# Performance work log

Hardware: AMD Instinct MI355X
Metric: run time of the kernel (lower is better)

## Reference

```python
import jax, jax.numpy as jnp
import numpy as np

B, T, I, H, V = 128, 1024, 256, 512, 32000


def setup_inputs() -> dict:
    key = jax.random.key(0)
    ks = jax.random.split(key, 16)
    s = lambda fan_in: 1.0 / np.sqrt(fan_in)
    return {
        "x": jax.random.normal(ks[0], (B, 1, I), jnp.float32),
        "hp": jax.random.normal(ks[1], (1, B, H), jnp.float32),
        "cp": jax.random.normal(ks[2], (1, B, H), jnp.float32),
        "op": jax.random.normal(ks[3], (B, H), jnp.float32),
        "encoder_outputs": jax.random.normal(ks[4], (B, T, H), jnp.float32),
        # LSTM params (PyTorch gate order: i, f, g, o)
        "W_ih": jax.random.uniform(ks[5], (4 * H, I + H), jnp.float32, -s(H), s(H)),
        "W_hh": jax.random.uniform(ks[6], (4 * H, H), jnp.float32, -s(H), s(H)),
        "b_ih": jax.random.uniform(ks[7], (4 * H,), jnp.float32, -s(H), s(H)),
        "b_hh": jax.random.uniform(ks[8], (4 * H,), jnp.float32, -s(H), s(H)),
        # Bahdanau attention (all bias-free)
        "Wq": jax.random.uniform(ks[9], (H, H), jnp.float32, -s(H), s(H)),
        "Wm": jax.random.uniform(ks[10], (H, H), jnp.float32, -s(H), s(H)),
        "Wa": jax.random.uniform(ks[11], (1, H), jnp.float32, -s(H), s(H)),
        # output layers (bias-free)
        "Wo": jax.random.uniform(ks[12], (H, 2 * H), jnp.float32, -s(2 * H), s(2 * H)),
        "Wout": jax.random.uniform(ks[13], (V, H), jnp.float32, -s(H), s(H)),
    }


def reference(x, hp, cp, op, encoder_outputs, W_ih, W_hh, b_ih, b_hh, Wq, Wm, Wa, Wo, Wout):
    h = H  # hidden size
    # --- single-step LSTM (seq len 1) ---
    lstm_in = jnp.concatenate([x[:, 0, :], op], axis=-1)  # (B, I+H)
    gates = lstm_in @ W_ih.T + hp[0] @ W_hh.T + (b_ih + b_hh)  # (B, 4H)
    i_g = jax.nn.sigmoid(gates[:, 0 * h:1 * h])
    f_g = jax.nn.sigmoid(gates[:, 1 * h:2 * h])
    g_g = jnp.tanh(gates[:, 2 * h:3 * h])
    o_g = jax.nn.sigmoid(gates[:, 3 * h:4 * h])
    cn = f_g * cp[0] + i_g * g_g            # (B, H)
    hn = o_g * jnp.tanh(cn)                 # (B, H)

    # --- Bahdanau additive attention ---
    q = hn @ Wq.T                            # (B, H)
    k = jnp.einsum('bth,gh->btg', encoder_outputs, Wm)  # (B, T, H)
    scores = jnp.tanh(q[:, None, :] + k) @ Wa[0]         # (B, T)
    weights = jax.nn.softmax(scores, axis=1)             # softmax over time
    context = jnp.einsum('bt,btm->bm', weights, encoder_outputs)  # (B, H)

    # --- output head ---
    o_in = jnp.concatenate([hn, context], axis=1)  # (B, 2H)
    on = jnp.tanh(o_in @ Wo.T)                     # (B, H)
    output = jax.nn.log_softmax(on @ Wout.T, axis=1)  # (B, V)

    return (output, (hn[None], cn[None]), on, weights[:, None, :])
```

## Files before the change

### kernel.cpp

```cpp
#include <hip/hip_runtime.h>

#define B_ 128
#define T_ 1024
#define I_ 256
#define H_ 512
#define V_ 32000

typedef float  float4v __attribute__((ext_vector_type(4)));
typedef short  short8  __attribute__((ext_vector_type(8)));

__device__ __forceinline__ unsigned short f2bf(float f){
  unsigned int u = __float_as_uint(f);
  u += 0x7fffu + ((u >> 16) & 1u);
  return (unsigned short)(u >> 16);
}
__device__ __forceinline__ ushort4 f2bf4(float4 v){
  ushort4 u; u.x=f2bf(v.x); u.y=f2bf(v.y); u.z=f2bf(v.z); u.w=f2bf(v.w); return u;
}
__device__ __forceinline__ unsigned int cvt_pk_bf16(float lo, float hi){
  unsigned int r;
  asm volatile("v_cvt_pk_bf16_f32 %0, %1, %2" : "=v"(r) : "v"(lo), "v"(hi));
  return r;
}
__device__ __forceinline__ float fast_tanh(float x){
  float e = __expf(2.f*x);
  return 1.f - __fdividef(2.f, e + 1.f);
}
__device__ __forceinline__ float fast_sig(float x){
  return __fdividef(1.f, 1.f + __expf(-x));
}

__global__ void conv_bf16(const float4* __restrict__ src, ushort4* __restrict__ dst, int n4){
  int i = blockIdx.x*256 + threadIdx.x;
  if (i < n4) dst[i] = f2bf4(src[i]);
}

__device__ __forceinline__ const float* fetch_in(int mode, const float* a0, const float* a1,
                                                 const float* a2, int b, int k){
  if (mode == 0){
    if (k < 256)  return a0 + b*256 + k;
    if (k < 768)  return a1 + b*512 + (k-256);
    return a2 + b*512 + (k-768);
  }
  if (mode == 1) return a0 + b*512 + k;
  if (k < 512)   return a0 + b*512 + k;
  return a1 + b*512 + (k-512);
}
__device__ __forceinline__ const float* fetch_w(int mode, const float* w0, const float* w1,
                                                int n, int k){
  if (mode == 0){
    if (k < 768) return w0 + (size_t)n*768 + k;
    return w1 + (size_t)n*512 + (k-768);
  }
  if (mode == 1) return w0 + (size_t)n*512 + k;
  return w0 + (size_t)n*1024 + k;
}

__global__ void sgemm_acc(int mode,
    const float* __restrict__ a0, const float* __restrict__ a1, const float* __restrict__ a2,
    const float* __restrict__ w0, const float* __restrict__ w1,
    float* __restrict__ out, int N, int kchunk)
{
  __shared__ float inp_s[64*132];
  __shared__ float w_s[64*40];
  int tid = threadIdx.x;
  int nt = blockIdx.x, kid = blockIdx.y;
  int bg = tid & 31, ng = tid >> 5;
  int sb = tid >> 1, skof = (tid & 1)*32;
  int wn = tid & 31, wkg = tid >> 5;
  float acc[4][4] = {};
  int substeps = kchunk >> 6;

  for (int s = 0; s < substeps; ++s){
    int ks = kid*kchunk + s*64;
    __syncthreads();
    {
      const float* src = fetch_in(mode, a0, a1, a2, sb, ks + skof);
      #pragma unroll
      for (int j8 = 0; j8 < 8; ++j8){
        float4 v = ((const float4*)src)[j8];
        int kk = skof + j8*4;
        inp_s[(kk+0)*132 + sb] = v.x;
        inp_s[(kk+1)*132 + sb] = v.y;
        inp_s[(kk+2)*132 + sb] = v.z;
        inp_s[(kk+3)*132 + sb] = v.w;
      }
      int nglob = nt*32 + wn;
      const float* wsrc = fetch_w(mode, w0, w1, nglob, ks + wkg*8);
      float4 v0 = ((const float4*)wsrc)[0];
      float4 v1 = ((const float4*)wsrc)[1];
      int kk = wkg*8;
      w_s[(kk+0)*40 + wn] = v0.x;  w_s[(kk+1)*40 + wn] = v0.y;
      w_s[(kk+2)*40 + wn] = v0.z;  w_s[(kk+3)*40 + wn] = v0.w;
      w_s[(kk+4)*40 + wn] = v1.x;  w_s[(kk+5)*40 + wn] = v1.y;
      w_s[(kk+6)*40 + wn] = v1.z;  w_s[(kk+7)*40 + wn] = v1.w;
    }
    __syncthreads();
    #pragma unroll 4
    for (int k = 0; k < 64; ++k){
      float4v vb = *(const float4v*)&inp_s[k*132 + bg*4];
      float4v vw = *(const float4v*)&w_s[k*40 + ng*4];
      #pragma unroll
      for (int i = 0; i < 4; ++i)
        #pragma unroll
        for (int j = 0; j < 4; ++j)
          acc[i][j] = fmaf(vb[i], vw[j], acc[i][j]);
    }
  }
  #pragma unroll
  for (int i = 0; i < 4; ++i)
    #pragma unroll
    for (int j = 0; j < 4; ++j)
      atomicAdd(&out[(size_t)(bg*4+i)*N + nt*32 + ng*4 + j], acc[i][j]);
}

__global__ void lstm_act(const float* __restrict__ gates,
    const float* __restrict__ bih, const float* __restrict__ bhh,
    const float* __restrict__ cp, float* __restrict__ hn_out, float* __restrict__ cn_out)
{
  int i = blockIdx.x*256 + threadIdx.x;
  int b = i >> 9, h = i & 511;
  const float* g = gates + (size_t)b*2048;
  float g0 = g[h]      + bih[h]      + bhh[h];
  float g1 = g[512+h]  + bih[512+h]  + bhh[512+h];
  float g2 = g[1024+h] + bih[1024+h] + bhh[1024+h];
  float g3 = g[1536+h] + bih[1536+h] + bhh[1536+h];
  float ig = fast_sig(g0), fg = fast_sig(g1);
  float gg = fast_tanh(g2), og = fast_sig(g3);
  float cv = fg*cp[i] + ig*gg;
  float hv = og*fast_tanh(cv);
  cn_out[i] = cv;
  hn_out[i] = hv;
}

__global__ __launch_bounds__(256, 4) void attn_gemm(
    const float* __restrict__ enc, const unsigned short* __restrict__ wmbf,
    const float* __restrict__ q, const float* __restrict__ wa,
    float* __restrict__ sp)
{
  __shared__ unsigned short As[2][4096];
  __shared__ unsigned short Bs[2][4096];
  __shared__ float sred[2][128];

  int tid = threadIdx.x;
  int blk = blockIdx.x;
  int nc = blk & 3, tc = (blk >> 2) & 7, b = blk >> 5;
  int tbase = tc*128, n0 = nc*128;
  int w = tid >> 6, lane = tid & 63;
  int wm = w >> 1, wn = w & 1;
  int c = lane & 15, q4 = lane >> 4;

  float4v acc[4][4];
  #pragma unroll
  for (int i = 0; i < 4; ++i)
    #pragma unroll
    for (int j = 0; j < 4; ++j) acc[i][j] = (float4v)0.f;

  int sr = tid >> 1, sh = tid & 1;
  const float* asrc = enc + ((size_t)(b*1024 + tbase + sr))*512 + sh*16;
  const unsigned short* bsrc = wmbf + (size_t)(n0 + sr)*512 + sh*16;
  int srp = sr >> 1, sodd = sr & 1;
  int wo0 = srp*64 + ((sodd*4 + sh*2    ) ^ (srp & 7))*8;
  int wo1 = srp*64 + ((sodd*4 + sh*2 + 1) ^ (srp & 7))*8;

  int a_off[4], b_off[4];
  #pragma unroll
  for (int mi = 0; mi < 4; ++mi){
    int r = wm*64 + mi*16 + c;
    a_off[mi] = (r >> 1)*64 + (((r & 1)*4 + q4) ^ ((r >> 1) & 7))*8;
  }
  #pragma unroll
  for (int ni = 0; ni < 4; ++ni){
    int r = wn*64 + ni*16 + c;
    b_off[ni] = (r >> 1)*64 + (((r & 1)*4 + q4) ^ ((r >> 1) & 7))*8;
  }

  float4 a0, a1, a2, a3;
  uint4 bv0, bv1;

  a0 = ((const float4*)asrc)[0]; a1 = ((const float4*)asrc)[1];
  a2 = ((const float4*)asrc)[2]; a3 = ((const float4*)asrc)[3];
  bv0 = *(const uint4*)(bsrc);   bv1 = *(const uint4*)(bsrc + 8);
  {
    uint4 ca, cb;
    ca.x = cvt_pk_bf16(a0.x, a0.y); ca.y = cvt_pk_bf16(a0.z, a0.w);
    ca.z = cvt_pk_bf16(a1.x, a1.y); ca.w = cvt_pk_bf16(a1.z, a1.w);
    cb.x = cvt_pk_bf16(a2.x, a2.y); cb.y = cvt_pk_bf16(a2.z, a2.w);
    cb.z = cvt_pk_bf16(a3.x, a3.y); cb.w = cvt_pk_bf16(a3.z, a3.w);
    *(uint4*)&As[0][wo0] = ca; *(uint4*)&As[0][wo1] = cb;
    *(uint4*)&Bs[0][wo0] = bv0; *(uint4*)&Bs[0][wo1] = bv1;
  }
  a0 = ((const float4*)(asrc + 32))[0]; a1 = ((const float4*)(asrc + 32))[1];
  a2 = ((const float4*)(asrc + 32))[2]; a3 = ((const float4*)(asrc + 32))[3];
  bv0 = *(const uint4*)(bsrc + 32);     bv1 = *(const uint4*)(bsrc + 40);
  __syncthreads();

  for (int ks = 0; ks < 16; ++ks){
    int cur = ks & 1;
    if (ks < 15){
      uint4 ca, cb;
      ca.x = cvt_pk_bf16(a0.x, a0.y); ca.y = cvt_pk_bf16(a0.z, a0.w);
      ca.z = cvt_pk_bf16(a1.x, a1.y); ca.w = cvt_pk_bf16(a1.z, a1.w);
      cb.x = cvt_pk_bf16(a2.x, a2.y); cb.y = cvt_pk_bf16(a2.z, a2.w);
      cb.z = cvt_pk_bf16(a3.x, a3.y); cb.w = cvt_pk_bf16(a3.z, a3.w);
      *(uint4*)&As[cur^1][wo0] = ca; *(uint4*)&As[cur^1][wo1] = cb;
      *(uint4*)&Bs[cur^1][wo0] = bv0; *(uint4*)&Bs[cur^1][wo1] = bv1;
      if (ks < 14){
        int k0 = (ks + 2)*32;
        a0 = ((const float4*)(asrc + k0))[0]; a1 = ((const float4*)(asrc + k0))[1];
        a2 = ((const float4*)(asrc + k0))[2]; a3 = ((const float4*)(asrc + k0))[3];
        bv0 = *(const uint4*)(bsrc + k0);     bv1 = *(const uint4*)(bsrc + k0 + 8);
      }
    }
    short8 af[4];
    #pragma unroll
    for (int mi = 0; mi < 4; ++mi)
      af[mi] = *(const short8*)&As[cur][a_off[mi]];
    #pragma unroll
    for (int ni = 0; ni < 4; ++ni){
      short8 bf = *(const short8*)&Bs[cur][b_off[ni]];
      #pragma unroll
      for (int mi = 0; mi < 4; ++mi)
        acc[mi][ni] = __builtin_amdgcn_mfma_f32_16x16x32_bf16(af[mi], bf, acc[mi][ni], 0, 0, 0);
    }
    __syncthreads();
  }

  float qv[4], wv[4];
  #pragma unroll
  for (int ni = 0; ni < 4; ++ni){
    int n = n0 + wn*64 + ni*16 + c;
    qv[ni] = q[b*512 + n]; wv[ni] = wa[n];
  }
  #pragma unroll
  for (int mi = 0; mi < 4; ++mi){
    #pragma unroll
    for (int r = 0; r < 4; ++r){
      float v = 0.f;
      #pragma unroll
      for (int ni = 0; ni < 4; ++ni)
        v += wv[ni] * fast_tanh(qv[ni] + acc[mi][ni][r]);
      v += __shfl_xor(v, 1); v += __shfl_xor(v, 2);
      v += __shfl_xor(v, 4); v += __shfl_xor(v, 8);
      if (c == 0) sred[wn][wm*64 + mi*16 + q4*4 + r] = v;
    }
  }
  __syncthreads();
  if (tid < 128)
    sp[nc*131072 + b*1024 + tbase + tid] = sred[0][tid] + sred[1][tid];
}

__global__ __launch_bounds__(1024) void attn_softmax(const float* __restrict__ sp,
                                                     float* __restrict__ wf)
{
  __shared__ float red[16];
  int b = blockIdx.x, tid = threadIdx.x;
  int w = tid >> 6, lane = tid & 63;
  float s = sp[b*1024 + tid] + sp[131072 + b*1024 + tid]
          + sp[262144 + b*1024 + tid] + sp[393216 + b*1024 + tid];
  float m = s;
  m = fmaxf(m, __shfl_xor(m, 32)); m = fmaxf(m, __shfl_xor(m, 16));
  m = fmaxf(m, __shfl_xor(m, 8));  m = fmaxf(m, __shfl_xor(m, 4));
  m = fmaxf(m, __shfl_xor(m, 2));  m = fmaxf(m, __shfl_xor(m, 1));
  if (lane == 0) red[w] = m;
  __syncthreads();
  float M = red[0];
  #pragma unroll
  for (int i = 1; i < 16; ++i) M = fmaxf(M, red[i]);
  __syncthreads();
  float p = __expf(s - M);
  float t = p;
  t += __shfl_xor(t, 32); t += __shfl_xor(t, 16); t += __shfl_xor(t, 8);
  t += __shfl_xor(t, 4);  t += __shfl_xor(t, 2);  t += __shfl_xor(t, 1);
  if (lane == 0) red[w] = t;
  __syncthreads();
  float L = 0.f;
  #pragma unroll
  for (int i = 0; i < 16; ++i) L += red[i];
  wf[b*1024 + tid] = p * __fdividef(1.f, L);
}

__global__ __launch_bounds__(512) void attn_ctx(const float* __restrict__ wgt,
    const float* __restrict__ enc, float* __restrict__ ctx)
{
  __shared__ float wl[128];
  int blk = blockIdx.x;
  int b = blk >> 3, tc = blk & 7;
  int tid = threadIdx.x;
  if (tid < 128) wl[tid] = wgt[b*1024 + tc*128 + tid];
  __syncthreads();
  const float* ep = enc + ((size_t)(b*1024 + tc*128))*512 + tid;
  float a = 0.f;
  #pragma unroll 8
  for (int t2 = 0; t2 < 128; ++t2)
    a = fmaf(wl[t2], ep[(size_t)t2*512], a);
  atomicAdd(&ctx[b*512 + tid], a);
}

__global__ void tanh_act(const float* __restrict__ in, float* __restrict__ out){
  int i = blockIdx.x*256 + threadIdx.x;
  out[i] = fast_tanh(in[i]);
}

__global__ void head_gemm(const float* __restrict__ onv, const float* __restrict__ wout,
                          float* __restrict__ outp)
{
  __shared__ unsigned short As[128*40];
  __shared__ unsigned short Bs[128*40];
  int tid = threadIdx.x;
  int n0 = blockIdx.x * 128;
  int w = tid >> 6, lane = tid & 63;
  int wm = w >> 1, wn = w & 1;
  int c = lane & 15, q4 = lane >> 4;
  float4v acc[4][4];
  #pragma unroll
  for (int i = 0; i < 4; ++i)
    #pragma unroll
    for (int j = 0; j < 4; ++j) acc[i][j] = (float4v)0.f;

  int row = tid >> 1, kof = (tid & 1)*16;
  const float* sa = onv + (size_t)row*512 + kof;
  const float* sb = wout + (size_t)(n0 + row)*512 + kof;

  for (int ks = 0; ks < 16; ++ks){
    int k0 = ks*32;
    __syncthreads();
    #pragma unroll
    for (int j = 0; j < 4; ++j){
      float4 va = *(const float4*)(sa + k0 + j*4);
      *(ushort4*)&As[row*40 + kof + j*4] = f2bf4(va);
      float4 vb = *(const float4*)(sb + k0 + j*4);
      *(ushort4*)&Bs[row*40 + kof + j*4] = f2bf4(vb);
    }
    __syncthreads();
    short8 af[4];
    #pragma unroll
    for (int mi = 0; mi < 4; ++mi)
      af[mi] = *(const short8*)&As[(wm*64 + mi*16 + c)*40 + q4*8];
    #pragma unroll
    for (int ni = 0; ni < 4; ++ni){
      short8 bf = *(const short8*)&Bs[(wn*64 + ni*16 + c)*40 + q4*8];
      #pragma unroll
      for (int mi = 0; mi < 4; ++mi)
        acc[mi][ni] = __builtin_amdgcn_mfma_f32_16x16x32_bf16(af[mi], bf, acc[mi][ni], 0, 0, 0);
    }
  }
  #pragma unroll
  for (int mi = 0; mi < 4; ++mi)
    #pragma unroll
    for (int ni = 0; ni < 4; ++ni)
      #pragma unroll
      for (int r = 0; r < 4; ++r){
        int m = wm*64 + mi*16 + q4*4 + r;
        int n = n0 + wn*64 + ni*16 + c;
        outp[(size_t)m*32000 + n] = acc[mi][ni][r];
      }
}

__global__ void lse_rows(const float* __restrict__ outp, float* __restrict__ lse){
  __shared__ float rm[4], rs[4];
  int b = blockIdx.x, tid = threadIdx.x;
  int w = tid >> 6, lane = tid & 63;
  const float* row = outp + (size_t)b*32000;
  float m = -1e30f, s = 0.f;
  for (int v = tid; v < 32000; v += 256){
    float x = row[v];
    if (x > m){ s = s*__expf(m - x) + 1.f; m = x; }
    else s += __expf(x - m);
  }
  for (int off = 32; off; off >>= 1){
    float mo = __shfl_xor(m, off), so = __shfl_xor(s, off);
    float M2 = fmaxf(m, mo);
    s = s*__expf(m - M2) + so*__expf(mo - M2);
    m = M2;
  }
  if (lane == 0){ rm[w] = m; rs[w] = s; }
  __syncthreads();
  if (tid == 0){
    float M2 = fmaxf(fmaxf(rm[0], rm[1]), fmaxf(rm[2], rm[3]));
    float S = rs[0]*__expf(rm[0]-M2) + rs[1]*__expf(rm[1]-M2)
            + rs[2]*__expf(rm[2]-M2) + rs[3]*__expf(rm[3]-M2);
    lse[b] = M2 + __logf(S);
  }
}

__global__ void sub_lse(float4* outp4, const float* __restrict__ lse){
  int i = blockIdx.x*256 + threadIdx.x;
  int b = i / 8000;
  float l = lse[b];
  float4 v = outp4[i];
  v.x -= l; v.y -= l; v.z -= l; v.w -= l;
  outp4[i] = v;
}

extern "C" void kernel_launch(void* const* d_in, const int* in_sizes, int n_in,
                              void* d_out, int out_size, void* d_ws, size_t ws_size,
                              hipStream_t stream)
{
  (void)in_sizes; (void)n_in; (void)out_size; (void)ws_size;
  const float* x    = (const float*)d_in[0];
  const float* hp   = (const float*)d_in[1];
  const float* cp   = (const float*)d_in[2];
  const float* op   = (const float*)d_in[3];
  const float* enc  = (const float*)d_in[4];
  const float* Wih  = (const float*)d_in[5];
  const float* Whh  = (const float*)d_in[6];
  const float* bih  = (const float*)d_in[7];
  const float* bhh  = (const float*)d_in[8];
  const float* Wq   = (const float*)d_in[9];
  const float* Wm   = (const float*)d_in[10];
  const float* Wa   = (const float*)d_in[11];
  const float* Wo   = (const float*)d_in[12];
  const float* Wout = (const float*)d_in[13];
  float* out = (float*)d_out;

  float* ws = (float*)d_ws;
  float* gates   = ws + 0;
  float* qbuf    = ws + 262144;
  unsigned short* wmbf = (unsigned short*)(ws + 327680);
  float* spb     = ws + 458752;
  float* ctxb    = ws + 983040;
  float* oaccb   = ws + 1048576;
  float* lseb    = ws + 1114112;

  float* out_logits = out;
  float* out_hn = out + 4096000;
  float* out_cn = out + 4161536;
  float* out_on = out + 4227072;
  float* out_w  = out + 4292608;

  hipMemsetAsync(gates, 0, (size_t)(262144 + 65536)*sizeof(float), stream);
  hipMemsetAsync(ctxb, 0, (size_t)(65536 + 65536)*sizeof(float), stream);

  conv_bf16<<<256, 256, 0, stream>>>((const float4*)Wm, (ushort4*)wmbf, 65536);
  sgemm_acc<<<dim3(64, 4), 256, 0, stream>>>(0, x, op, hp, Wih, Whh, gates, 2048, 320);
  lstm_act<<<256, 256, 0, stream>>>(gates, bih, bhh, cp, out_hn, out_cn);
  sgemm_acc<<<dim3(16, 8), 256, 0, stream>>>(1, out_hn, nullptr, nullptr, Wq, nullptr, qbuf, 512, 64);
  attn_gemm<<<4096, 256, 0, stream>>>(enc, wmbf, qbuf, Wa, spb);
  attn_softmax<<<128, 1024, 0, stream>>>(spb, out_w);
  attn_ctx<<<1024, 512, 0, stream>>>(out_w, enc, ctxb);
  sgemm_acc<<<dim3(16, 8), 256, 0, stream>>>(2, out_hn, ctxb, nullptr, Wo, nullptr, oaccb, 512, 128);
  tanh_act<<<256, 256, 0, stream>>>(oaccb, out_on);
  head_gemm<<<250, 256, 0, stream>>>(out_on, Wout, out_logits);
  lse_rows<<<128, 256, 0, stream>>>(out_logits, lseb);
  sub_lse<<<4000, 256, 0, stream>>>((float4*)out_logits, lseb);
}
```

Before: 771.4 us.

## Fuse attention softmax with context, pipeline head GEMM, fuse LSE, swizzle attention blocks

Remaps attention GEMM blocks so the four column chunks of a tile land on the same XCD, reuses the A tile LDS for the reduction scratch and raises the occupancy hint. Merges the softmax into the context kernel, with each block recomputing the row softmax. Adds a bf16 copy of the output activation so the head GEMM loads bf16 A directly, double-buffers it with swizzled LDS and uses 64-wide column tiles. Folds the log-sum-exp and its subtraction into one kernel to remove one pass over the logits. The trade-off is redundant softmax work per block and possible register pressure from the higher occupancy target.

```diff
diff --git a/kernel.cpp b/kernel.cpp
--- a/kernel.cpp
+++ b/kernel.cpp
@@ -133,18 +133,20 @@
   hn_out[i] = hv;
 }
 
-__global__ __launch_bounds__(256, 4) void attn_gemm(
+__global__ __launch_bounds__(256, 5) void attn_gemm(
     const float* __restrict__ enc, const unsigned short* __restrict__ wmbf,
     const float* __restrict__ q, const float* __restrict__ wa,
     float* __restrict__ sp)
 {
   __shared__ unsigned short As[2][4096];
   __shared__ unsigned short Bs[2][4096];
-  __shared__ float sred[2][128];
 
   int tid = threadIdx.x;
   int blk = blockIdx.x;
-  int nc = blk & 3, tc = (blk >> 2) & 7, b = blk >> 5;
+  int xcd = blk & 7, slot = blk >> 3;
+  int tile = xcd + 8*(slot >> 2);
+  int nc = slot & 3;
+  int b = tile >> 3, tc = tile & 7;
   int tbase = tc*128, n0 = nc*128;
   int w = tid >> 6, lane = tid & 63;
   int wm = w >> 1, wn = w & 1;
@@ -226,6 +228,7 @@
     __syncthreads();
   }
 
+  float* sred = (float*)&As[0][0];
   float qv[4], wv[4];
   #pragma unroll
   for (int ni = 0; ni < 4; ++ni){
@@ -242,23 +245,29 @@
         v += wv[ni] * fast_tanh(qv[ni] + acc[mi][ni][r]);
       v += __shfl_xor(v, 1); v += __shfl_xor(v, 2);
       v += __shfl_xor(v, 4); v += __shfl_xor(v, 8);
-      if (c == 0) sred[wn][wm*64 + mi*16 + q4*4 + r] = v;
+      if (c == 0) sred[wn*128 + wm*64 + mi*16 + q4*4 + r] = v;
     }
   }
   __syncthreads();
   if (tid < 128)
-    sp[nc*131072 + b*1024 + tbase + tid] = sred[0][tid] + sred[1][tid];
-}
-
-__global__ __launch_bounds__(1024) void attn_softmax(const float* __restrict__ sp,
-                                                     float* __restrict__ wf)
-{
-  __shared__ float red[16];
-  int b = blockIdx.x, tid = threadIdx.x;
+    sp[nc*131072 + b*1024 + tbase + tid] = sred[tid] + sred[128 + tid];
+}
+
+__global__ __launch_bounds__(512) void attn_sm_ctx(const float* __restrict__ sp,
+    const float* __restrict__ enc, float* __restrict__ wf, float* __restrict__ ctx)
+{
+  __shared__ float sv[1024];
+  __shared__ float red[8], red2[8];
+  int blk = blockIdx.x;
+  int b = blk >> 3, tc = blk & 7;
+  int tid = threadIdx.x;
   int w = tid >> 6, lane = tid & 63;
-  float s = sp[b*1024 + tid] + sp[131072 + b*1024 + tid]
-          + sp[262144 + b*1024 + tid] + sp[393216 + b*1024 + tid];
-  float m = s;
+  int t1 = tid + 512;
+  float s0 = sp[b*1024 + tid] + sp[131072 + b*1024 + tid]
+           + sp[262144 + b*1024 + tid] + sp[393216 + b*1024 + tid];
+  float s1 = sp[b*1024 + t1] + sp[131072 + b*1024 + t1]
+           + sp[262144 + b*1024 + t1] + sp[393216 + b*1024 + t1];
+  float m = fmaxf(s0, s1);
   m = fmaxf(m, __shfl_xor(m, 32)); m = fmaxf(m, __shfl_xor(m, 16));
   m = fmaxf(m, __shfl_xor(m, 8));  m = fmaxf(m, __shfl_xor(m, 4));
   m = fmaxf(m, __shfl_xor(m, 2));  m = fmaxf(m, __shfl_xor(m, 1));
@@ -266,104 +275,138 @@
   __syncthreads();
   float M = red[0];
   #pragma unroll
-  for (int i = 1; i < 16; ++i) M = fmaxf(M, red[i]);
-  __syncthreads();
-  float p = __expf(s - M);
-  float t = p;
+  for (int i = 1; i < 8; ++i) M = fmaxf(M, red[i]);
+  float p0 = __expf(s0 - M), p1 = __expf(s1 - M);
+  float t = p0 + p1;
   t += __shfl_xor(t, 32); t += __shfl_xor(t, 16); t += __shfl_xor(t, 8);
   t += __shfl_xor(t, 4);  t += __shfl_xor(t, 2);  t += __shfl_xor(t, 1);
-  if (lane == 0) red[w] = t;
+  if (lane == 0) red2[w] = t;
   __syncthreads();
   float L = 0.f;
   #pragma unroll
-  for (int i = 0; i < 16; ++i) L += red[i];
-  wf[b*1024 + tid] = p * __fdividef(1.f, L);
-}
-
-__global__ __launch_bounds__(512) void attn_ctx(const float* __restrict__ wgt,
-    const float* __restrict__ enc, float* __restrict__ ctx)
-{
-  __shared__ float wl[128];
-  int blk = blockIdx.x;
-  int b = blk >> 3, tc = blk & 7;
-  int tid = threadIdx.x;
-  if (tid < 128) wl[tid] = wgt[b*1024 + tc*128 + tid];
-  __syncthreads();
-  const float* ep = enc + ((size_t)(b*1024 + tc*128))*512 + tid;
+  for (int i = 0; i < 8; ++i) L += red2[i];
+  float invL = __fdividef(1.f, L);
+  sv[tid] = p0*invL;
+  sv[t1]  = p1*invL;
+  __syncthreads();
+  int tbase = tc*128;
+  if (tid < 128) wf[b*1024 + tbase + tid] = sv[tbase + tid];
+  const float* ep = enc + ((size_t)(b*1024 + tbase))*512 + tid;
   float a = 0.f;
   #pragma unroll 8
   for (int t2 = 0; t2 < 128; ++t2)
-    a = fmaf(wl[t2], ep[(size_t)t2*512], a);
+    a = fmaf(sv[tbase + t2], ep[(size_t)t2*512], a);
   atomicAdd(&ctx[b*512 + tid], a);
 }
 
-__global__ void tanh_act(const float* __restrict__ in, float* __restrict__ out){
+__global__ void tanh_act(const float* __restrict__ in, float* __restrict__ out,
+                         unsigned short* __restrict__ outbf){
   int i = blockIdx.x*256 + threadIdx.x;
-  out[i] = fast_tanh(in[i]);
-}
-
-__global__ void head_gemm(const float* __restrict__ onv, const float* __restrict__ wout,
-                          float* __restrict__ outp)
-{
-  __shared__ unsigned short As[128*40];
-  __shared__ unsigned short Bs[128*40];
+  float v = fast_tanh(in[i]);
+  out[i] = v;
+  outbf[i] = f2bf(v);
+}
+
+__global__ __launch_bounds__(256) void head_gemm(const unsigned short* __restrict__ onbf,
+    const float* __restrict__ wout, float* __restrict__ outp)
+{
+  __shared__ unsigned short As[2][4096];
+  __shared__ unsigned short Bs[2][2048];
   int tid = threadIdx.x;
-  int n0 = blockIdx.x * 128;
+  int n0 = blockIdx.x * 64;
   int w = tid >> 6, lane = tid & 63;
   int wm = w >> 1, wn = w & 1;
   int c = lane & 15, q4 = lane >> 4;
-  float4v acc[4][4];
+
+  float4v acc[4][2];
   #pragma unroll
   for (int i = 0; i < 4; ++i)
     #pragma unroll
-    for (int j = 0; j < 4; ++j) acc[i][j] = (float4v)0.f;
-
-  int row = tid >> 1, kof = (tid & 1)*16;
-  const float* sa = onv + (size_t)row*512 + kof;
-  const float* sb = wout + (size_t)(n0 + row)*512 + kof;
+    for (int j = 0; j < 2; ++j) acc[i][j] = (float4v)0.f;
+
+  int sr = tid >> 1, sh = tid & 1;
+  const unsigned short* asrc = onbf + (size_t)sr*512 + sh*16;
+  int srp = sr >> 1, sodd = sr & 1;
+  int awo0 = srp*64 + ((sodd*4 + sh*2    ) ^ (srp & 7))*8;
+  int awo1 = srp*64 + ((sodd*4 + sh*2 + 1) ^ (srp & 7))*8;
+  int rb = tid >> 2, jb = tid & 3;
+  const float* bsrc = wout + (size_t)(n0 + rb)*512 + jb*8;
+  int rbp = rb >> 1, rbo = rb & 1;
+  int bwo = rbp*64 + ((rbo*4 + jb) ^ (rbp & 7))*8;
+
+  int a_off[4], b_off[2];
+  #pragma unroll
+  for (int mi = 0; mi < 4; ++mi){
+    int r = wm*64 + mi*16 + c;
+    a_off[mi] = (r >> 1)*64 + (((r & 1)*4 + q4) ^ ((r >> 1) & 7))*8;
+  }
+  #pragma unroll
+  for (int ni = 0; ni < 2; ++ni){
+    int r = wn*32 + ni*16 + c;
+    b_off[ni] = (r >> 1)*64 + (((r & 1)*4 + q4) ^ ((r >> 1) & 7))*8;
+  }
+
+  uint4 pa0, pa1;
+  float4 pb0, pb1;
+  pa0 = ((const uint4*)asrc)[0]; pa1 = ((const uint4*)asrc)[1];
+  pb0 = ((const float4*)bsrc)[0]; pb1 = ((const float4*)bsrc)[1];
+  {
+    *(uint4*)&As[0][awo0] = pa0; *(uint4*)&As[0][awo1] = pa1;
+    uint4 cb;
+    cb.x = cvt_pk_bf16(pb0.x, pb0.y); cb.y = cvt_pk_bf16(pb0.z, pb0.w);
+    cb.z = cvt_pk_bf16(pb1.x, pb1.y); cb.w = cvt_pk_bf16(pb1.z, pb1.w);
+    *(uint4*)&Bs[0][bwo] = cb;
+  }
+  pa0 = ((const uint4*)(asrc + 32))[0]; pa1 = ((const uint4*)(asrc + 32))[1];
+  pb0 = ((const float4*)(bsrc + 32))[0]; pb1 = ((const float4*)(bsrc + 32))[1];
+  __syncthreads();
 
   for (int ks = 0; ks < 16; ++ks){
-    int k0 = ks*32;
-    __syncthreads();
-    #pragma unroll
-    for (int j = 0; j < 4; ++j){
-      float4 va = *(const float4*)(sa + k0 + j*4);
-      *(ushort4*)&As[row*40 + kof + j*4] = f2bf4(va);
-      float4 vb = *(const float4*)(sb + k0 + j*4);
-      *(ushort4*)&Bs[row*40 + kof + j*4] = f2bf4(vb);
-    }
-    __syncthreads();
+    int cur = ks & 1;
+    if (ks < 15){
+      *(uint4*)&As[cur^1][awo0] = pa0; *(uint4*)&As[cur^1][awo1] = pa1;
+      uint4 cb;
+      cb.x = cvt_pk_bf16(pb0.x, pb0.y); cb.y = cvt_pk_bf16(pb0.z, pb0.w);
+      cb.z = cvt_pk_bf16(pb1.x, pb1.y); cb.w = cvt_pk_bf16(pb1.z, pb1.w);
+      *(uint4*)&Bs[cur^1][bwo] = cb;
+      if (ks < 14){
+        int k0 = (ks + 2)*32;
+        pa0 = ((const uint4*)(asrc + k0))[0]; pa1 = ((const uint4*)(asrc + k0))[1];
+        pb0 = ((const float4*)(bsrc + k0))[0]; pb1 = ((const float4*)(bsrc + k0))[1];
+      }
+    }
     short8 af[4];
     #pragma unroll
     for (int mi = 0; mi < 4; ++mi)
-      af[mi] = *(const short8*)&As[(wm*64 + mi*16 + c)*40 + q4*8];
-    #pragma unroll
-    for (int ni = 0; ni < 4; ++ni){
-      short8 bf = *(const short8*)&Bs[(wn*64 + ni*16 + c)*40 + q4*8];
+      af[mi] = *(const short8*)&As[cur][a_off[mi]];
+    #pragma unroll
+    for (int ni = 0; ni < 2; ++ni){
+      short8 bf = *(const short8*)&Bs[cur][b_off[ni]];
       #pragma unroll
       for (int mi = 0; mi < 4; ++mi)
         acc[mi][ni] = __builtin_amdgcn_mfma_f32_16x16x32_bf16(af[mi], bf, acc[mi][ni], 0, 0, 0);
     }
+    __syncthreads();
   }
   #pragma unroll
   for (int mi = 0; mi < 4; ++mi)
     #pragma unroll
-    for (int ni = 0; ni < 4; ++ni)
+    for (int ni = 0; ni < 2; ++ni)
       #pragma unroll
       for (int r = 0; r < 4; ++r){
         int m = wm*64 + mi*16 + q4*4 + r;
-        int n = n0 + wn*64 + ni*16 + c;
+        int n = n0 + wn*32 + ni*16 + c;
         outp[(size_t)m*32000 + n] = acc[mi][ni][r];
       }
 }
 
-__global__ void lse_rows(const float* __restrict__ outp, float* __restrict__ lse){
-  __shared__ float rm[4], rs[4];
+__global__ __launch_bounds__(1024) void lse_fused(float* __restrict__ outp){
+  __shared__ float rm[16], rs[16];
   int b = blockIdx.x, tid = threadIdx.x;
   int w = tid >> 6, lane = tid & 63;
-  const float* row = outp + (size_t)b*32000;
+  float* row = outp + (size_t)b*32000;
   float m = -1e30f, s = 0.f;
-  for (int v = tid; v < 32000; v += 256){
+  for (int v = tid; v < 32000; v += 1024){
     float x = row[v];
     if (x > m){ s = s*__expf(m - x) + 1.f; m = x; }
     else s += __expf(x - m);
@@ -376,21 +419,15 @@
   }
   if (lane == 0){ rm[w] = m; rs[w] = s; }
   __syncthreads();
-  if (tid == 0){
-    float M2 = fmaxf(fmaxf(rm[0], rm[1]), fmaxf(rm[2], rm[3]));
-    float S = rs[0]*__expf(rm[0]-M2) + rs[1]*__expf(rm[1]-M2)
-            + rs[2]*__expf(rm[2]-M2) + rs[3]*__expf(rm[3]-M2);
-    lse[b] = M2 + __logf(S);
-  }
-}
-
-__global__ void sub_lse(float4* outp4, const float* __restrict__ lse){
-  int i = blockIdx.x*256 + threadIdx.x;
-  int b = i / 8000;
-  float l = lse[b];
-  float4 v = outp4[i];
-  v.x -= l; v.y -= l; v.z -= l; v.w -= l;
-  outp4[i] = v;
+  float M = rm[0];
+  #pragma unroll
+  for (int i = 1; i < 16; ++i) M = fmaxf(M, rm[i]);
+  float S = 0.f;
+  #pragma unroll
+  for (int i = 0; i < 16; ++i) S += rs[i]*__expf(rm[i] - M);
+  float l = M + __logf(S);
+  for (int v = tid; v < 32000; v += 1024)
+    row[v] -= l;
 }
 
 extern "C" void kernel_launch(void* const* d_in, const int* in_sizes, int n_in,
@@ -421,7 +458,7 @@
   float* spb     = ws + 458752;
   float* ctxb    = ws + 983040;
   float* oaccb   = ws + 1048576;
-  float* lseb    = ws + 1114112;
+  unsigned short* onbf = (unsigned short*)(ws + 1114112);
 
   float* out_logits = out;
   float* out_hn = out + 4096000;
@@ -437,11 +474,9 @@
   lstm_act<<<256, 256, 0, stream>>>(gates, bih, bhh, cp, out_hn, out_cn);
   sgemm_acc<<<dim3(16, 8), 256, 0, stream>>>(1, out_hn, nullptr, nullptr, Wq, nullptr, qbuf, 512, 64);
   attn_gemm<<<4096, 256, 0, stream>>>(enc, wmbf, qbuf, Wa, spb);
-  attn_softmax<<<128, 1024, 0, stream>>>(spb, out_w);
-  attn_ctx<<<1024, 512, 0, stream>>>(out_w, enc, ctxb);
+  attn_sm_ctx<<<1024, 512, 0, stream>>>(spb, enc, out_w, ctxb);
   sgemm_acc<<<dim3(16, 8), 256, 0, stream>>>(2, out_hn, ctxb, nullptr, Wo, nullptr, oaccb, 512, 128);
-  tanh_act<<<256, 256, 0, stream>>>(oaccb, out_on);
-  head_gemm<<<250, 256, 0, stream>>>(out_on, Wout, out_logits);
-  lse_rows<<<128, 256, 0, stream>>>(out_logits, lseb);
-  sub_lse<<<4000, 256, 0, stream>>>((float4*)out_logits, lseb);
-}
+  tanh_act<<<256, 256, 0, stream>>>(oaccb, out_on, onbf);
+  head_gemm<<<500, 256, 0, stream>>>(onbf, Wout, out_logits);
+  lse_fused<<<128, 1024, 0, stream>>>(out_logits);
+}
```

New measurement: 757.9 us. Within noise of the previous version (-1.8%).
